# Kernel tuning notes

Measured on AMD Instinct MI355X. Metric: run time of the kernel, lower is better.

The kernel has to match this reference:

```python
import jax, jax.numpy as jnp
import numpy as np

N = 128   # system size (number of sequential RNN steps)
B = 8192  # batch of samples
H = 128   # hidden units per layer (units=[128,128])
D = 2     # input_dim (spin up/down one-hot)


def setup_inputs() -> dict:
    key = jax.random.key(0)
    ks = jax.random.split(key, 11)
    s = 1.0 / np.sqrt(H)  # torch nn.RNNCell/Linear default U(-1/sqrt(H), 1/sqrt(H))
    bits = jax.random.randint(ks[0], (N, B), 0, D)
    samples = jax.nn.one_hot(bits, D, dtype=jnp.float32)  # (N, B, D) one-hot spins
    u = lambda k, shp: jax.random.uniform(k, shp, jnp.float32, -s, s)
    return {
        "samples": samples,
        "W_ih0": u(ks[1], (H, D)), "b_ih0": u(ks[2], (H,)),
        "W_hh0": u(ks[3], (H, H)), "b_hh0": u(ks[4], (H,)),
        "W_ih1": u(ks[5], (H, H)), "b_ih1": u(ks[6], (H,)),
        "W_hh1": u(ks[7], (H, H)), "b_hh1": u(ks[8], (H,)),
        "W_dense": u(ks[9], (D, H)), "b_dense": u(ks[10], (D,)),
    }


def reference(samples, W_ih0, b_ih0, W_hh0, b_hh0,
              W_ih1, b_ih1, W_hh1, b_hh1, W_dense, b_dense):
    # Faithful jax port of RNN_wavefunction.log_prob:
    # p_t = <softmax(dense(h1_t)), s_t>; returns sum_t log p_t with shape (1, B).
    # For one-hot s_t, log(sum(prob*s_t)) == sum(s_t * log_softmax(logits)) (stable form).
    Bsz = samples.shape[1]
    # input at step t is the sampled spin from step t-1; zeros at t=0
    inputs = jnp.concatenate(
        [jnp.zeros((1, Bsz, D), samples.dtype), samples[:-1]], axis=0)
    h0 = jnp.zeros((Bsz, H), samples.dtype)
    h1 = jnp.zeros((Bsz, H), samples.dtype)

    def step(carry, xs):
        h0, h1 = carry
        x_t, s_t = xs  # x_t: (B, D) prev spin one-hot, s_t: (B, D) current spin
        # nn.RNNCell: h' = tanh(x W_ih^T + b_ih + h W_hh^T + b_hh)
        h0 = jnp.tanh(x_t @ W_ih0.T + b_ih0 + h0 @ W_hh0.T + b_hh0)
        h1 = jnp.tanh(h0 @ W_ih1.T + b_ih1 + h1 @ W_hh1.T + b_hh1)
        logits = h1 @ W_dense.T + b_dense           # (B, 2)
        logp = jax.nn.log_softmax(logits, axis=-1)
        lp_t = jnp.sum(logp * s_t, axis=-1)          # (B,) = log p(s_t)
        return (h0, h1), lp_t

    _, lps = jax.lax.scan(step, (h0, h1), (inputs, samples))  # lps: (N, B)
    return jnp.sum(lps, axis=0, keepdims=True)  # (1, B), matches torch keepdim=True
```

## Files before the change

kernel.cpp:

```cpp
#include <hip/hip_runtime.h>
#include <hip/hip_bf16.h>


#define NSTEP 128
#define BTOT  8192
#define HID   128
#define MB    16
#define NBLK  (BTOT / MB)
#define NTHR  256

typedef __attribute__((ext_vector_type(8))) short bf16x8;
typedef __attribute__((ext_vector_type(4))) float f32x4;
typedef __attribute__((ext_vector_type(2))) float f32x2;
typedef __attribute__((ext_vector_type(2))) unsigned uint32x2;

__device__ __forceinline__ short f2bf(float v) {
    unsigned u = __builtin_bit_cast(unsigned, v);
    u += 0x7FFFu + ((u >> 16) & 1u);
    return (short)(u >> 16);
}
__device__ __forceinline__ unsigned cvt2bf(float a, float b) {
    __hip_bfloat162 h2 = __float22bfloat162_rn(make_float2(a, b));
    unsigned u; __builtin_memcpy(&u, &h2, sizeof(u));
    return u;
}
__device__ __forceinline__ f32x2 tanh2(f32x2 x) {
    f32x2 z = x * 2.885390081777927f;
    float e0 = __builtin_exp2f(z.x);
    float e1 = __builtin_exp2f(z.y);
    f32x2 d = {e0 + 1.0f, e1 + 1.0f};
    float r = __builtin_amdgcn_rcpf(d.x * d.y);
    f32x2 inv = {r * d.y, r * d.x};
    return inv * -2.0f + 1.0f;
}

__global__ __launch_bounds__(NTHR, 2) void rnn_wf_kernel(
    const float* __restrict__ samples,
    const float* __restrict__ Wih0,
    const float* __restrict__ bih0,
    const float* __restrict__ Whh0,
    const float* __restrict__ bhh0,
    const float* __restrict__ Wih1,
    const float* __restrict__ bih1,
    const float* __restrict__ Whh1,
    const float* __restrict__ bhh1,
    const float* __restrict__ Wd,
    const float* __restrict__ bd,
    float* __restrict__ out)
{
    __shared__ short sH0[2][MB * HID];
    __shared__ short sH1[2][MB * HID];
    __shared__ unsigned sMask[NSTEP];
    __shared__ float sLd[NSTEP * 17];

    const int tid  = threadIdx.x;
    const int b0   = blockIdx.x * MB;
    const int w    = tid >> 6;
    const int lane = tid & 63;
    const int q    = lane >> 4;
    const int c    = lane & 15;
    const int nb   = w * 32;

    if (tid < NSTEP) {
        unsigned msk = 0;
        #pragma unroll
        for (int m = 0; m < MB; ++m) {
            float e1 = samples[((size_t)tid * BTOT + b0 + m) * 2 + 1];
            if (e1 > 0.5f) msk |= (1u << m);
        }
        sMask[tid] = msk;
    }

    bf16x8 fhh0[2][4], fih1[2][4], fhh1[2][4];
    #pragma unroll
    for (int nt = 0; nt < 2; ++nt) {
        const int nn = nb + nt * 16 + c;
        #pragma unroll
        for (int kb = 0; kb < 4; ++kb) {
            const int off = nn * HID + kb * 32 + q * 8;
            bf16x8 v0, v1, v2;
            #pragma unroll
            for (int j = 0; j < 8; ++j) {
                v0[j] = f2bf(Whh0[off + j]);
                v1[j] = f2bf(Wih1[off + j]);
                v2[j] = f2bf(Whh1[off + j]);
            }
            fhh0[nt][kb] = v0; fih1[nt][kb] = v1; fhh1[nt][kb] = v2;
        }
    }
    bf16x8 fwd[4];
    #pragma unroll
    for (int kb = 0; kb < 4; ++kb) {
        bf16x8 v;
        #pragma unroll
        for (int j = 0; j < 8; ++j)
            v[j] = (c < 2) ? f2bf(Wd[c * HID + kb * 32 + q * 8 + j]) : (short)0;
        fwd[kb] = v;
    }
    f32x4 pA0, pA1, pB0, pB1, b0v0, b0v1, b1v0, b1v1;
    #pragma unroll
    for (int r = 0; r < 4; ++r) {
        const int n0 = nb + q * 4 + r;
        const int n1 = n0 + 16;
        const float bb0 = bih0[n0] + bhh0[n0];
        const float bb1 = bih0[n1] + bhh0[n1];
        b0v0[r] = bb0;                    b0v1[r] = bb1;
        pA0[r] = bb0 + Wih0[n0 * 2 + 0];  pA1[r] = bb1 + Wih0[n1 * 2 + 0];
        pB0[r] = bb0 + Wih0[n0 * 2 + 1];  pB1[r] = bb1 + Wih0[n1 * 2 + 1];
        b1v0[r] = bih1[n0] + bhh1[n0];    b1v1[r] = bih1[n1] + bhh1[n1];
    }
    const f32x4 bdv = {bd[0], bd[1], 0.f, 0.f};

    int ra[4];
    #pragma unroll
    for (int kb = 0; kb < 4; ++kb)
        ra[kb] = c * HID + (((kb * 4 + q) ^ c) << 3);
    const int wa0 = c * HID + (((4 * w + (q >> 1)) ^ c) << 3) + ((q & 1) << 2);
    const int wa1 = c * HID + (((4 * w + 2 + (q >> 1)) ^ c) << 3) + ((q & 1) << 2);

    bool bmPrev = false;

    auto storeH = [&](short* buf, const f32x4& a0, const f32x4& a1) {
        f32x2 t00 = tanh2((f32x2){a0[0], a0[1]});
        f32x2 t01 = tanh2((f32x2){a0[2], a0[3]});
        f32x2 t10 = tanh2((f32x2){a1[0], a1[1]});
        f32x2 t11 = tanh2((f32x2){a1[2], a1[3]});
        uint32x2 v0 = {cvt2bf(t00.x, t00.y), cvt2bf(t01.x, t01.y)};
        uint32x2 v1 = {cvt2bf(t10.x, t10.y), cvt2bf(t11.x, t11.y)};
        *reinterpret_cast<uint32x2*>(&buf[wa0]) = v0;
        *reinterpret_cast<uint32x2*>(&buf[wa1]) = v1;
    };

    __syncthreads();
    storeH(sH0[1], b0v0, b0v1);
    __syncthreads();

    {
        const bool bmIn = (sMask[0] >> c) & 1u;
        bf16x8 f0[4];
        #pragma unroll
        for (int kb = 0; kb < 4; ++kb)
            f0[kb] = *reinterpret_cast<const bf16x8*>(&sH0[1][ra[kb]]);
        f32x4 a00 = __builtin_amdgcn_mfma_f32_16x16x32_bf16(fhh0[0][0], f0[0], bmIn ? pB0 : pA0, 0, 0, 0);
        f32x4 a01 = __builtin_amdgcn_mfma_f32_16x16x32_bf16(fhh0[1][0], f0[0], bmIn ? pB1 : pA1, 0, 0, 0);
        f32x4 a10 = __builtin_amdgcn_mfma_f32_16x16x32_bf16(fih1[0][0], f0[0], b1v0, 0, 0, 0);
        f32x4 a11 = __builtin_amdgcn_mfma_f32_16x16x32_bf16(fih1[1][0], f0[0], b1v1, 0, 0, 0);
        #pragma unroll
        for (int kb = 1; kb < 4; ++kb) {
            a00 = __builtin_amdgcn_mfma_f32_16x16x32_bf16(fhh0[0][kb], f0[kb], a00, 0, 0, 0);
            a01 = __builtin_amdgcn_mfma_f32_16x16x32_bf16(fhh0[1][kb], f0[kb], a01, 0, 0, 0);
            a10 = __builtin_amdgcn_mfma_f32_16x16x32_bf16(fih1[0][kb], f0[kb], a10, 0, 0, 0);
            a11 = __builtin_amdgcn_mfma_f32_16x16x32_bf16(fih1[1][kb], f0[kb], a11, 0, 0, 0);
        }
        storeH(sH0[0], a00, a01);
        storeH(sH1[0], a10, a11);
        bmPrev = bmIn;
        __syncthreads();
    }

    auto stepMain = [&](int i, const short* r0, const short* r1,
                        short* w0b, short* w1b) {
        const bool bmIn = (sMask[i - 1] >> c) & 1u;
        bf16x8 f0[4], f1[4];
        #pragma unroll
        for (int kb = 0; kb < 4; ++kb) {
            f0[kb] = *reinterpret_cast<const bf16x8*>(&r0[ra[kb]]);
            f1[kb] = *reinterpret_cast<const bf16x8*>(&r1[ra[kb]]);
        }
        f32x4 a00 = __builtin_amdgcn_mfma_f32_16x16x32_bf16(fhh0[0][0], f0[0], bmIn ? pB0 : pA0, 0, 0, 0);
        f32x4 a01 = __builtin_amdgcn_mfma_f32_16x16x32_bf16(fhh0[1][0], f0[0], bmIn ? pB1 : pA1, 0, 0, 0);
        f32x4 a10 = __builtin_amdgcn_mfma_f32_16x16x32_bf16(fhh1[0][0], f1[0], b1v0, 0, 0, 0);
        f32x4 a11 = __builtin_amdgcn_mfma_f32_16x16x32_bf16(fhh1[1][0], f1[0], b1v1, 0, 0, 0);
        #pragma unroll
        for (int kb = 1; kb < 4; ++kb) {
            a00 = __builtin_amdgcn_mfma_f32_16x16x32_bf16(fhh0[0][kb], f0[kb], a00, 0, 0, 0);
            a01 = __builtin_amdgcn_mfma_f32_16x16x32_bf16(fhh0[1][kb], f0[kb], a01, 0, 0, 0);
            a10 = __builtin_amdgcn_mfma_f32_16x16x32_bf16(fhh1[0][kb], f1[kb], a10, 0, 0, 0);
            a11 = __builtin_amdgcn_mfma_f32_16x16x32_bf16(fhh1[1][kb], f1[kb], a11, 0, 0, 0);
        }
        #pragma unroll
        for (int kb = 0; kb < 4; ++kb) {
            a10 = __builtin_amdgcn_mfma_f32_16x16x32_bf16(fih1[0][kb], f0[kb], a10, 0, 0, 0);
            a11 = __builtin_amdgcn_mfma_f32_16x16x32_bf16(fih1[1][kb], f0[kb], a11, 0, 0, 0);
        }
        if (w == 0) {
            f32x4 aL = __builtin_amdgcn_mfma_f32_16x16x32_bf16(fwd[0], f1[0], bdv, 0, 0, 0);
            #pragma unroll
            for (int kb = 1; kb < 4; ++kb)
                aL = __builtin_amdgcn_mfma_f32_16x16x32_bf16(fwd[kb], f1[kb], aL, 0, 0, 0);
            if (q == 0)
                sLd[(i - 2) * 17 + c] = bmPrev ? (aL[0] - aL[1]) : (aL[1] - aL[0]);
        }
        bmPrev = bmIn;
        storeH(w0b, a00, a01);
        storeH(w1b, a10, a11);
        __syncthreads();
    };

    for (int i = 2; i < NSTEP; i += 2) {
        stepMain(i,     sH0[0], sH1[0], sH0[1], sH1[1]);
        stepMain(i + 1, sH0[1], sH1[1], sH0[0], sH1[0]);
    }

    {
        bf16x8 f0[4], f1[4];
        #pragma unroll
        for (int kb = 0; kb < 4; ++kb) {
            f0[kb] = *reinterpret_cast<const bf16x8*>(&sH0[0][ra[kb]]);
            f1[kb] = *reinterpret_cast<const bf16x8*>(&sH1[0][ra[kb]]);
        }
        f32x4 a10 = __builtin_amdgcn_mfma_f32_16x16x32_bf16(fhh1[0][0], f1[0], b1v0, 0, 0, 0);
        f32x4 a11 = __builtin_amdgcn_mfma_f32_16x16x32_bf16(fhh1[1][0], f1[0], b1v1, 0, 0, 0);
        #pragma unroll
        for (int kb = 1; kb < 4; ++kb) {
            a10 = __builtin_amdgcn_mfma_f32_16x16x32_bf16(fhh1[0][kb], f1[kb], a10, 0, 0, 0);
            a11 = __builtin_amdgcn_mfma_f32_16x16x32_bf16(fhh1[1][kb], f1[kb], a11, 0, 0, 0);
        }
        #pragma unroll
        for (int kb = 0; kb < 4; ++kb) {
            a10 = __builtin_amdgcn_mfma_f32_16x16x32_bf16(fih1[0][kb], f0[kb], a10, 0, 0, 0);
            a11 = __builtin_amdgcn_mfma_f32_16x16x32_bf16(fih1[1][kb], f0[kb], a11, 0, 0, 0);
        }
        if (w == 0) {
            f32x4 aL = __builtin_amdgcn_mfma_f32_16x16x32_bf16(fwd[0], f1[0], bdv, 0, 0, 0);
            #pragma unroll
            for (int kb = 1; kb < 4; ++kb)
                aL = __builtin_amdgcn_mfma_f32_16x16x32_bf16(fwd[kb], f1[kb], aL, 0, 0, 0);
            if (q == 0)
                sLd[126 * 17 + c] = bmPrev ? (aL[0] - aL[1]) : (aL[1] - aL[0]);
        }
        storeH(sH1[1], a10, a11);
        __syncthreads();
    }
    if (w == 0) {
        f32x4 aL;
        {
            bf16x8 f1 = *reinterpret_cast<const bf16x8*>(&sH1[1][ra[0]]);
            aL = __builtin_amdgcn_mfma_f32_16x16x32_bf16(fwd[0], f1, bdv, 0, 0, 0);
        }
        #pragma unroll
        for (int kb = 1; kb < 4; ++kb) {
            bf16x8 f1 = *reinterpret_cast<const bf16x8*>(&sH1[1][ra[kb]]);
            aL = __builtin_amdgcn_mfma_f32_16x16x32_bf16(fwd[kb], f1, aL, 0, 0, 0);
        }
        if (q == 0) {
            const bool bit = (sMask[NSTEP - 1] >> c) & 1u;
            sLd[127 * 17 + c] = bit ? (aL[0] - aL[1]) : (aL[1] - aL[0]);
        }
    }
    __syncthreads();

    {
        const int s = tid >> 4;
        const int k = tid & 15;
        float acc = 0.0f;
        #pragma unroll
        for (int j = 0; j < 8; ++j) {
            const float x = sLd[(j * 16 + k) * 17 + s];
            const float ed = __builtin_exp2f(x * 1.4426950408889634f);
            acc -= 0.6931471805599453f * __builtin_log2f(1.0f + ed);
        }
        #pragma unroll
        for (int off = 1; off < 16; off <<= 1)
            acc += __shfl_xor(acc, off, 64);
        if (k == 0)
            out[b0 + s] = acc;
    }
}

extern "C" void kernel_launch(void* const* d_in, const int* in_sizes, int n_in,
                              void* d_out, int out_size, void* d_ws, size_t ws_size,
                              hipStream_t stream) {
    rnn_wf_kernel<<<NBLK, NTHR, 0, stream>>>(
        (const float*)d_in[0],
        (const float*)d_in[1],
        (const float*)d_in[2],
        (const float*)d_in[3],
        (const float*)d_in[4],
        (const float*)d_in[5],
        (const float*)d_in[6],
        (const float*)d_in[7],
        (const float*)d_in[8],
        (const float*)d_in[9],
        (const float*)d_in[10],
        (float*)d_out);
}
```

Baseline: 258.6 us.

## Move bias and dense weights to LDS and rotate logit work across waves

Per-thread bias vectors and dense-layer bf16 fragments are no longer held in registers. They are staged once in shared memory and reloaded from LDS each step, which frees VGPRs under the launch bound of 2 blocks per SM. The per-step logit MFMA chain now rotates across the four waves (w == i&3) instead of always running on wave 0, so the extra work per step is spread evenly. The cost is extra LDS reads on every step.

Result: faster. 245.1 us (-5.2%).

```diff
diff --git a/kernel.cpp b/kernel.cpp
--- a/kernel.cpp
+++ b/kernel.cpp
@@ -52,6 +52,8 @@
     __shared__ short sH1[2][MB * HID];
     __shared__ unsigned sMask[NSTEP];
     __shared__ float sLd[NSTEP * 17];
+    __shared__ __attribute__((aligned(16))) float sBias[4 * HID];
+    __shared__ __attribute__((aligned(16))) short sFwd[4 * 64 * 8];
 
     const int tid  = threadIdx.x;
     const int b0   = blockIdx.x * MB;
@@ -69,6 +71,21 @@
             if (e1 > 0.5f) msk |= (1u << m);
         }
         sMask[tid] = msk;
+    }
+    if (tid < HID) {
+        const float bb = bih0[tid] + bhh0[tid];
+        sBias[tid]       = bb + Wih0[tid * 2 + 0];
+        sBias[128 + tid] = bb + Wih0[tid * 2 + 1];
+        sBias[256 + tid] = bih1[tid] + bhh1[tid];
+        sBias[384 + tid] = bb;
+    }
+    {
+        const int kb = tid >> 6, l = tid & 63, cc = l & 15, qq = l >> 4;
+        bf16x8 v;
+        #pragma unroll
+        for (int j = 0; j < 8; ++j)
+            v[j] = (cc < 2) ? f2bf(Wd[cc * HID + kb * 32 + qq * 8 + j]) : (short)0;
+        *reinterpret_cast<bf16x8*>(&sFwd[(kb * 64 + l) * 8]) = v;
     }
 
     bf16x8 fhh0[2][4], fih1[2][4], fhh1[2][4];
@@ -88,28 +105,7 @@
             fhh0[nt][kb] = v0; fih1[nt][kb] = v1; fhh1[nt][kb] = v2;
         }
     }
-    bf16x8 fwd[4];
-    #pragma unroll
-    for (int kb = 0; kb < 4; ++kb) {
-        bf16x8 v;
-        #pragma unroll
-        for (int j = 0; j < 8; ++j)
-            v[j] = (c < 2) ? f2bf(Wd[c * HID + kb * 32 + q * 8 + j]) : (short)0;
-        fwd[kb] = v;
-    }
-    f32x4 pA0, pA1, pB0, pB1, b0v0, b0v1, b1v0, b1v1;
-    #pragma unroll
-    for (int r = 0; r < 4; ++r) {
-        const int n0 = nb + q * 4 + r;
-        const int n1 = n0 + 16;
-        const float bb0 = bih0[n0] + bhh0[n0];
-        const float bb1 = bih0[n1] + bhh0[n1];
-        b0v0[r] = bb0;                    b0v1[r] = bb1;
-        pA0[r] = bb0 + Wih0[n0 * 2 + 0];  pA1[r] = bb1 + Wih0[n1 * 2 + 0];
-        pB0[r] = bb0 + Wih0[n0 * 2 + 1];  pB1[r] = bb1 + Wih0[n1 * 2 + 1];
-        b1v0[r] = bih1[n0] + bhh1[n0];    b1v1[r] = bih1[n1] + bhh1[n1];
-    }
-    const f32x4 bdv = {bd[0], bd[1], 0.f, 0.f};
+    const float bd0 = bd[0], bd1 = bd[1];
 
     int ra[4];
     #pragma unroll
@@ -117,6 +113,7 @@
         ra[kb] = c * HID + (((kb * 4 + q) ^ c) << 3);
     const int wa0 = c * HID + (((4 * w + (q >> 1)) ^ c) << 3) + ((q & 1) << 2);
     const int wa1 = c * HID + (((4 * w + 2 + (q >> 1)) ^ c) << 3) + ((q & 1) << 2);
+    const int ib  = nb + q * 4;
 
     bool bmPrev = false;
 
@@ -132,21 +129,28 @@
     };
 
     __syncthreads();
-    storeH(sH0[1], b0v0, b0v1);
+
+    {
+        f32x4 c0 = *reinterpret_cast<const f32x4*>(&sBias[384 + ib]);
+        f32x4 c1 = *reinterpret_cast<const f32x4*>(&sBias[384 + ib + 16]);
+        storeH(sH0[1], c0, c1);
+    }
     __syncthreads();
 
     {
         const bool bmIn = (sMask[0] >> c) & 1u;
+        const float* bp = bmIn ? (sBias + 128) : sBias;
+        f32x4 c00 = *reinterpret_cast<const f32x4*>(&bp[ib]);
+        f32x4 c01 = *reinterpret_cast<const f32x4*>(&bp[ib + 16]);
+        f32x4 c10 = *reinterpret_cast<const f32x4*>(&sBias[256 + ib]);
+        f32x4 c11 = *reinterpret_cast<const f32x4*>(&sBias[256 + ib + 16]);
         bf16x8 f0[4];
         #pragma unroll
         for (int kb = 0; kb < 4; ++kb)
             f0[kb] = *reinterpret_cast<const bf16x8*>(&sH0[1][ra[kb]]);
-        f32x4 a00 = __builtin_amdgcn_mfma_f32_16x16x32_bf16(fhh0[0][0], f0[0], bmIn ? pB0 : pA0, 0, 0, 0);
-        f32x4 a01 = __builtin_amdgcn_mfma_f32_16x16x32_bf16(fhh0[1][0], f0[0], bmIn ? pB1 : pA1, 0, 0, 0);
-        f32x4 a10 = __builtin_amdgcn_mfma_f32_16x16x32_bf16(fih1[0][0], f0[0], b1v0, 0, 0, 0);
-        f32x4 a11 = __builtin_amdgcn_mfma_f32_16x16x32_bf16(fih1[1][0], f0[0], b1v1, 0, 0, 0);
-        #pragma unroll
-        for (int kb = 1; kb < 4; ++kb) {
+        f32x4 a00 = c00, a01 = c01, a10 = c10, a11 = c11;
+        #pragma unroll
+        for (int kb = 0; kb < 4; ++kb) {
             a00 = __builtin_amdgcn_mfma_f32_16x16x32_bf16(fhh0[0][kb], f0[kb], a00, 0, 0, 0);
             a01 = __builtin_amdgcn_mfma_f32_16x16x32_bf16(fhh0[1][kb], f0[kb], a01, 0, 0, 0);
             a10 = __builtin_amdgcn_mfma_f32_16x16x32_bf16(fih1[0][kb], f0[kb], a10, 0, 0, 0);
@@ -161,18 +165,19 @@
     auto stepMain = [&](int i, const short* r0, const short* r1,
                         short* w0b, short* w1b) {
         const bool bmIn = (sMask[i - 1] >> c) & 1u;
+        const float* bp = bmIn ? (sBias + 128) : sBias;
+        f32x4 a00 = *reinterpret_cast<const f32x4*>(&bp[ib]);
+        f32x4 a01 = *reinterpret_cast<const f32x4*>(&bp[ib + 16]);
+        f32x4 a10 = *reinterpret_cast<const f32x4*>(&sBias[256 + ib]);
+        f32x4 a11 = *reinterpret_cast<const f32x4*>(&sBias[256 + ib + 16]);
         bf16x8 f0[4], f1[4];
         #pragma unroll
         for (int kb = 0; kb < 4; ++kb) {
             f0[kb] = *reinterpret_cast<const bf16x8*>(&r0[ra[kb]]);
             f1[kb] = *reinterpret_cast<const bf16x8*>(&r1[ra[kb]]);
         }
-        f32x4 a00 = __builtin_amdgcn_mfma_f32_16x16x32_bf16(fhh0[0][0], f0[0], bmIn ? pB0 : pA0, 0, 0, 0);
-        f32x4 a01 = __builtin_amdgcn_mfma_f32_16x16x32_bf16(fhh0[1][0], f0[0], bmIn ? pB1 : pA1, 0, 0, 0);
-        f32x4 a10 = __builtin_amdgcn_mfma_f32_16x16x32_bf16(fhh1[0][0], f1[0], b1v0, 0, 0, 0);
-        f32x4 a11 = __builtin_amdgcn_mfma_f32_16x16x32_bf16(fhh1[1][0], f1[0], b1v1, 0, 0, 0);
-        #pragma unroll
-        for (int kb = 1; kb < 4; ++kb) {
+        #pragma unroll
+        for (int kb = 0; kb < 4; ++kb) {
             a00 = __builtin_amdgcn_mfma_f32_16x16x32_bf16(fhh0[0][kb], f0[kb], a00, 0, 0, 0);
             a01 = __builtin_amdgcn_mfma_f32_16x16x32_bf16(fhh0[1][kb], f0[kb], a01, 0, 0, 0);
             a10 = __builtin_amdgcn_mfma_f32_16x16x32_bf16(fhh1[0][kb], f1[kb], a10, 0, 0, 0);
@@ -183,11 +188,13 @@
             a10 = __builtin_amdgcn_mfma_f32_16x16x32_bf16(fih1[0][kb], f0[kb], a10, 0, 0, 0);
             a11 = __builtin_amdgcn_mfma_f32_16x16x32_bf16(fih1[1][kb], f0[kb], a11, 0, 0, 0);
         }
-        if (w == 0) {
-            f32x4 aL = __builtin_amdgcn_mfma_f32_16x16x32_bf16(fwd[0], f1[0], bdv, 0, 0, 0);
+        if (w == (i & 3)) {
+            f32x4 aL = {bd0, bd1, 0.f, 0.f};
             #pragma unroll
-            for (int kb = 1; kb < 4; ++kb)
-                aL = __builtin_amdgcn_mfma_f32_16x16x32_bf16(fwd[kb], f1[kb], aL, 0, 0, 0);
+            for (int kb = 0; kb < 4; ++kb) {
+                bf16x8 fw = *reinterpret_cast<const bf16x8*>(&sFwd[(kb * 64 + lane) * 8]);
+                aL = __builtin_amdgcn_mfma_f32_16x16x32_bf16(fw, f1[kb], aL, 0, 0, 0);
+            }
             if (q == 0)
                 sLd[(i - 2) * 17 + c] = bmPrev ? (aL[0] - aL[1]) : (aL[1] - aL[0]);
         }
@@ -203,16 +210,16 @@
     }
 
     {
+        f32x4 a10 = *reinterpret_cast<const f32x4*>(&sBias[256 + ib]);
+        f32x4 a11 = *reinterpret_cast<const f32x4*>(&sBias[256 + ib + 16]);
         bf16x8 f0[4], f1[4];
         #pragma unroll
         for (int kb = 0; kb < 4; ++kb) {
             f0[kb] = *reinterpret_cast<const bf16x8*>(&sH0[0][ra[kb]]);
             f1[kb] = *reinterpret_cast<const bf16x8*>(&sH1[0][ra[kb]]);
         }
-        f32x4 a10 = __builtin_amdgcn_mfma_f32_16x16x32_bf16(fhh1[0][0], f1[0], b1v0, 0, 0, 0);
-        f32x4 a11 = __builtin_amdgcn_mfma_f32_16x16x32_bf16(fhh1[1][0], f1[0], b1v1, 0, 0, 0);
-        #pragma unroll
-        for (int kb = 1; kb < 4; ++kb) {
+        #pragma unroll
+        for (int kb = 0; kb < 4; ++kb) {
             a10 = __builtin_amdgcn_mfma_f32_16x16x32_bf16(fhh1[0][kb], f1[kb], a10, 0, 0, 0);
             a11 = __builtin_amdgcn_mfma_f32_16x16x32_bf16(fhh1[1][kb], f1[kb], a11, 0, 0, 0);
         }
@@ -222,26 +229,25 @@
             a11 = __builtin_amdgcn_mfma_f32_16x16x32_bf16(fih1[1][kb], f0[kb], a11, 0, 0, 0);
         }
         if (w == 0) {
-            f32x4 aL = __builtin_amdgcn_mfma_f32_16x16x32_bf16(fwd[0], f1[0], bdv, 0, 0, 0);
+            f32x4 aL = {bd0, bd1, 0.f, 0.f};
             #pragma unroll
-            for (int kb = 1; kb < 4; ++kb)
-                aL = __builtin_amdgcn_mfma_f32_16x16x32_bf16(fwd[kb], f1[kb], aL, 0, 0, 0);
+            for (int kb = 0; kb < 4; ++kb) {
+                bf16x8 fw = *reinterpret_cast<const bf16x8*>(&sFwd[(kb * 64 + lane) * 8]);
+                aL = __builtin_amdgcn_mfma_f32_16x16x32_bf16(fw, f1[kb], aL, 0, 0, 0);
+            }
             if (q == 0)
                 sLd[126 * 17 + c] = bmPrev ? (aL[0] - aL[1]) : (aL[1] - aL[0]);
         }
         storeH(sH1[1], a10, a11);
         __syncthreads();
     }
-    if (w == 0) {
-        f32x4 aL;
-        {
-            bf16x8 f1 = *reinterpret_cast<const bf16x8*>(&sH1[1][ra[0]]);
-            aL = __builtin_amdgcn_mfma_f32_16x16x32_bf16(fwd[0], f1, bdv, 0, 0, 0);
-        }
-        #pragma unroll
-        for (int kb = 1; kb < 4; ++kb) {
+    if (w == 1) {
+        f32x4 aL = {bd0, bd1, 0.f, 0.f};
+        #pragma unroll
+        for (int kb = 0; kb < 4; ++kb) {
             bf16x8 f1 = *reinterpret_cast<const bf16x8*>(&sH1[1][ra[kb]]);
-            aL = __builtin_amdgcn_mfma_f32_16x16x32_bf16(fwd[kb], f1, aL, 0, 0, 0);
+            bf16x8 fw = *reinterpret_cast<const bf16x8*>(&sFwd[(kb * 64 + lane) * 8]);
+            aL = __builtin_amdgcn_mfma_f32_16x16x32_bf16(fw, f1, aL, 0, 0, 0);
         }
         if (q == 0) {
             const bool bit = (sMask[NSTEP - 1] >> c) & 1u;
```
